# Kernel tuning notes

Measured on AMD Instinct MI355X. Metric: run time of the kernel, lower is better.

The kernel has to match this reference:

```python
import jax, jax.numpy as jnp
import numpy as np

KV_H, Q_H, ATT_H = 256, 256, 128
B, S, SQ = 2, 1024, 512

def setup_inputs() -> dict:
    key = jax.random.key(0)
    ks = jax.random.split(key, 8)
    sc = lambda d: 1.0 / np.sqrt(d)
    return {
        "attention_kv": jax.random.normal(ks[0], (B, S, KV_H), dtype=jnp.float32),
        "attention_query": jax.random.normal(ks[1], (B, SQ, Q_H), dtype=jnp.float32),
        "W_kv": jax.random.uniform(ks[2], (KV_H, ATT_H), jnp.float32, -sc(KV_H), sc(KV_H)),
        "b_kv": jax.random.uniform(ks[3], (ATT_H,), jnp.float32, -sc(KV_H), sc(KV_H)),
        "W_q": jax.random.uniform(ks[4], (Q_H, ATT_H), jnp.float32, -sc(Q_H), sc(Q_H)),
        "b_q": jax.random.uniform(ks[5], (ATT_H,), jnp.float32, -sc(Q_H), sc(Q_H)),
        "w_v": jax.random.uniform(ks[6], (ATT_H,), jnp.float32, -sc(ATT_H), sc(ATT_H)),
        "b_v": jax.random.uniform(ks[7], (), jnp.float32, -sc(ATT_H), sc(ATT_H)),
    }

def reference(attention_kv, attention_query, W_kv, b_kv, W_q, b_q, w_v, b_v):
    # proj_kv: (B, S, A); proj_q: (B, Sq, A)
    proj_kv = jnp.einsum('bsh,ha->bsa', attention_kv, W_kv) + b_kv
    proj_q = jnp.einsum('bqh,ha->bqa', attention_query, W_q) + b_q
    # broadcast add + tanh -> (B, Sq, S, A)
    hidden = jnp.tanh(proj_kv[:, None, :, :] + proj_q[:, :, None, :])
    # scalar score per (b, q, s)
    attention_score = jnp.einsum('bqsa,a->bqs', hidden, w_v) + b_v
    attention_weight = jax.nn.softmax(attention_score, axis=-1)
    # weighted sum over kv sequence -> (B, Sq, KV_H)
    attention_output = jnp.einsum('bqs,bsh->bqh', attention_weight, attention_kv)
    return attention_output, attention_weight
```

## Files before the change

### kernel.cpp

```cpp
#include <hip/hip_runtime.h>

#define NB   2
#define SKV  1024
#define NSQ  512
#define HIN  256
#define HA   128
#define NQ   (NB * NSQ)
#define NR   (NB * SKV)

#define KSC 2.8853900817779268f

typedef float v2f __attribute__((ext_vector_type(2)));
__device__ __forceinline__ v2f pkfma(v2f a, v2f b, v2f c) {
    return __builtin_elementwise_fma(a, b, c);
}

__global__ __launch_bounds__(256) void proj_kernel(
    const float* __restrict__ kv,  const float* __restrict__ qy,
    const float* __restrict__ Wkv, const float* __restrict__ bkv,
    const float* __restrict__ Wq,  const float* __restrict__ bq,
    float* __restrict__ ekT,
    float* __restrict__ eq)
{
    const int t = threadIdx.x;
    const int a = t & 127;
    const int g = __builtin_amdgcn_readfirstlane(t >> 7);
    const int blk = blockIdx.x;
    const bool is_q = blk >= 256;
    const int r0 = (is_q ? (blk - 256) : blk) * 8 + g * 4;
    const float* __restrict__ src = (is_q ? qy : kv) + (size_t)r0 * HIN;
    const float* __restrict__ W  = is_q ? Wq : Wkv;
    const float* __restrict__ bs = is_q ? bq : bkv;

    float ac0 = 0.f, ac1 = 0.f, ac2 = 0.f, ac3 = 0.f;
    #pragma unroll 8
    for (int h = 0; h < HIN; ++h) {
        const float w  = W[(size_t)h * HA + a];
        const float x0 = src[h];
        const float x1 = src[HIN + h];
        const float x2 = src[2 * HIN + h];
        const float x3 = src[3 * HIN + h];
        ac0 = fmaf(x0, w, ac0);
        ac1 = fmaf(x1, w, ac1);
        ac2 = fmaf(x2, w, ac2);
        ac3 = fmaf(x3, w, ac3);
    }
    const float bb = bs[a];
    const float o0 = __builtin_amdgcn_exp2f((ac0 + bb) * KSC);
    const float o1 = __builtin_amdgcn_exp2f((ac1 + bb) * KSC);
    const float o2 = __builtin_amdgcn_exp2f((ac2 + bb) * KSC);
    const float o3 = __builtin_amdgcn_exp2f((ac3 + bb) * KSC);
    if (!is_q) {
        float* __restrict__ d = ekT + (size_t)a * NR + r0;
        d[0] = o0; d[1] = o1; d[2] = o2; d[3] = o3;
    } else {
        eq[(size_t)(r0 + 0) * HA + a] = o0;
        eq[(size_t)(r0 + 1) * HA + a] = o1;
        eq[(size_t)(r0 + 2) * HA + a] = o2;
        eq[(size_t)(r0 + 3) * HA + a] = o3;
    }
}

__global__ __launch_bounds__(256) void score_kernel(
    const float* __restrict__ ekT,
    const float* __restrict__ eq,
    const float* __restrict__ wv,
    float* __restrict__ ew,
    float* __restrict__ ewT,
    float* __restrict__ Dp)
{
    __shared__ float dred[4][8];
    const int t = threadIdx.x;
    const int lane = t & 63, wid = t >> 6;
    const int blk = blockIdx.x;
    const int sq  = blk & 3;
    const int oct = blk >> 2;
    const int q0  = oct * 8;
    const int b   = q0 >> 9;
    const int s   = sq * 256 + t;
    const int srow = b * SKV + s;

    v2f acc[8];
    #pragma unroll
    for (int j = 0; j < 8; ++j) acc[j] = (v2f){0.f, 0.f};
    const v2f one = {1.f, 1.f};

    #pragma unroll 2
    for (int a4 = 0; a4 < 32; ++a4) {
        const float E0 = ekT[(size_t)(a4 * 4 + 0) * NR + srow];
        const float E1 = ekT[(size_t)(a4 * 4 + 1) * NR + srow];
        const float E2 = ekT[(size_t)(a4 * 4 + 2) * NR + srow];
        const float E3 = ekT[(size_t)(a4 * 4 + 3) * NR + srow];
        const float4 w4 = *(const float4*)(wv + a4 * 4);
        const v2f E01 = {E0, E1}, E23 = {E2, E3};
        const v2f w01 = {w4.x, w4.y}, w23 = {w4.z, w4.w};
        #pragma unroll
        for (int j = 0; j < 8; ++j) {
            const float4 qv = *(const float4*)(eq + (size_t)(q0 + j) * HA + a4 * 4);
            const v2f A = pkfma(E01, (v2f){qv.x, qv.y}, one);
            const v2f B = pkfma(E23, (v2f){qv.z, qv.w}, one);
            const v2f m = A * B;
            const float r = __builtin_amdgcn_rcpf(m.x * m.y);
            const v2f ts = (v2f){m.y, m.x} * (v2f){r, r};
            acc[j] = pkfma(w01, ts * B, acc[j]);
            acc[j] = pkfma(w23, ts * A, acc[j]);
        }
    }

    float ev[8];
    #pragma unroll
    for (int j = 0; j < 8; ++j) {
        ev[j] = __builtin_amdgcn_exp2f(-KSC * (acc[j].x + acc[j].y));
        ew[(size_t)(q0 + j) * SKV + s] = ev[j];
    }
    {
        float* __restrict__ wp = ewT + ((size_t)oct * SKV + s) * 8;
        *(float4*)(wp)     = make_float4(ev[0], ev[1], ev[2], ev[3]);
        *(float4*)(wp + 4) = make_float4(ev[4], ev[5], ev[6], ev[7]);
    }
    #pragma unroll
    for (int j = 0; j < 8; ++j) {
        float ss = ev[j];
        #pragma unroll
        for (int o = 32; o > 0; o >>= 1) ss += __shfl_down(ss, o);
        if (lane == 0) dred[wid][j] = ss;
    }
    __syncthreads();
    if (t < 8) {
        float d = dred[0][t] + dred[1][t] + dred[2][t] + dred[3][t];
        Dp[(size_t)sq * NQ + q0 + t] = d;
    }
}

__global__ __launch_bounds__(512) void out_kernel(
    const float* __restrict__ ewT,
    const float* __restrict__ kv,
    float* __restrict__ P)
{
    const int t = threadIdx.x;
    const int lane = t & 63;
    const int wu = __builtin_amdgcn_readfirstlane(t >> 6);
    const int blk = blockIdx.x;
    const int k  = blk & 3;
    const int gi = blk >> 2;
    const int q0 = gi * 16;
    const int b  = q0 >> 9;
    const int o0 = q0 >> 3;

    v2f acc[16][2];
    #pragma unroll
    for (int j = 0; j < 16; ++j) { acc[j][0] = (v2f){0.f, 0.f}; acc[j][1] = (v2f){0.f, 0.f}; }

    const int sbase = k * 256 + wu * 32;
    const float* __restrict__ kvb = kv + ((size_t)b * SKV + sbase) * HIN + lane * 4;
    const float* __restrict__ wA = ewT + ((size_t)o0 * SKV + sbase) * 8;
    const float* __restrict__ wB = ewT + ((size_t)(o0 + 1) * SKV + sbase) * 8;

    #pragma unroll 4
    for (int i = 0; i < 32; ++i) {
        const float4 v = *(const float4*)(kvb + (size_t)i * HIN);
        const v2f vlo = {v.x, v.y}, vhi = {v.z, v.w};
        const float4 a0 = *(const float4*)(wA + (size_t)i * 8);
        const float4 a1 = *(const float4*)(wA + (size_t)i * 8 + 4);
        const float4 b0 = *(const float4*)(wB + (size_t)i * 8);
        const float4 b1 = *(const float4*)(wB + (size_t)i * 8 + 4);
        const float wq[16] = {a0.x, a0.y, a0.z, a0.w, a1.x, a1.y, a1.z, a1.w,
                              b0.x, b0.y, b0.z, b0.w, b1.x, b1.y, b1.z, b1.w};
        #pragma unroll
        for (int j = 0; j < 16; ++j) {
            const v2f wj = {wq[j], wq[j]};
            acc[j][0] = pkfma(vlo, wj, acc[j][0]);
            acc[j][1] = pkfma(vhi, wj, acc[j][1]);
        }
    }
    float* __restrict__ Pp = P + (size_t)(k * 8 + wu) * ((size_t)NQ * HIN);
    #pragma unroll
    for (int j = 0; j < 16; ++j) {
        *(float4*)(Pp + (size_t)(q0 + j) * HIN + lane * 4) =
            make_float4(acc[j][0].x, acc[j][0].y, acc[j][1].x, acc[j][1].y);
    }
}

__global__ __launch_bounds__(256) void final_kernel(
    const float* __restrict__ ew,
    const float* __restrict__ Dp,
    const float* __restrict__ P,
    float* __restrict__ out)
{
    const int t = threadIdx.x;
    const int q = blockIdx.x;
    const float D = Dp[q] + Dp[NQ + q] + Dp[2 * NQ + q] + Dp[3 * NQ + q];
    const float rw = 1.0f / D;

    float* __restrict__ outw = out + (size_t)NQ * HIN;
    #pragma unroll
    for (int c = 0; c < 4; ++c) {
        const int s = c * 256 + t;
        outw[(size_t)q * SKV + s] = ew[(size_t)q * SKV + s] * rw;
    }
    float v = 0.f;
    #pragma unroll
    for (int p = 0; p < 32; ++p)
        v += P[(size_t)p * ((size_t)NQ * HIN) + (size_t)q * HIN + t];
    out[(size_t)q * HIN + t] = v * rw;
}

extern "C" void kernel_launch(void* const* d_in, const int* in_sizes, int n_in,
                              void* d_out, int out_size, void* d_ws, size_t ws_size,
                              hipStream_t stream) {
    (void)in_sizes; (void)n_in; (void)out_size; (void)ws_size;
    const float* kv  = (const float*)d_in[0];
    const float* qy  = (const float*)d_in[1];
    const float* Wkv = (const float*)d_in[2];
    const float* bkv = (const float*)d_in[3];
    const float* Wq  = (const float*)d_in[4];
    const float* bq  = (const float*)d_in[5];
    const float* wv  = (const float*)d_in[6];
    const float* bv  = (const float*)d_in[7];
    (void)bv;

    float* ekT = (float*)d_ws;
    float* eq  = ekT + 262144;
    float* ew  = eq  + 131072;
    float* ewT = ew  + 1048576;
    float* Dp  = ewT + 1048576;
    float* P   = Dp  + 4096;
    float* out = (float*)d_out;

    hipLaunchKernelGGL(proj_kernel,  dim3(384),  dim3(256), 0, stream,
                       kv, qy, Wkv, bkv, Wq, bq, ekT, eq);
    hipLaunchKernelGGL(score_kernel, dim3(512),  dim3(256), 0, stream,
                       ekT, eq, wv, ew, ewT, Dp);
    hipLaunchKernelGGL(out_kernel,   dim3(256),  dim3(512), 0, stream,
                       ewT, kv, P);
    hipLaunchKernelGGL(final_kernel, dim3(1024), dim3(256), 0, stream,
                       ew, Dp, P, out);
}
```

Before: 129.4 us.

## Fuse four attention stages into one cooperative kernel with grid syncs

Replaces the four separate launches (projection, score, weighted sum, final reduction) with a single cooperative kernel of 256 blocks of 1024 threads that uses grid.sync between phases. The work split is also reorganized: projection splits the hidden reduction across thread groups and combines the halves in shared memory, and the output stage reduces partials in shared memory so only two partial slices are written instead of thirty-two. The aim is to cut launch gaps and partial-sum traffic, at the cost of grid-wide barriers and only 256 large blocks, which may leave the GPU underoccupied.

```diff
diff --git a/kernel.cpp b/kernel.cpp
--- a/kernel.cpp
+++ b/kernel.cpp
@@ -1,12 +1,13 @@
 #include <hip/hip_runtime.h>
-
-#define NB   2
+#include <hip/hip_cooperative_groups.h>
+namespace cg = cooperative_groups;
+
 #define SKV  1024
 #define NSQ  512
 #define HIN  256
 #define HA   128
-#define NQ   (NB * NSQ)
-#define NR   (NB * SKV)
+#define NQ   1024
+#define NR   2048
 
 #define KSC 2.8853900817779268f
 
@@ -15,194 +16,213 @@
     return __builtin_elementwise_fma(a, b, c);
 }
 
-__global__ __launch_bounds__(256) void proj_kernel(
+__global__ __launch_bounds__(1024, 4) void fused_kernel(
     const float* __restrict__ kv,  const float* __restrict__ qy,
     const float* __restrict__ Wkv, const float* __restrict__ bkv,
     const float* __restrict__ Wq,  const float* __restrict__ bq,
+    const float* __restrict__ wv,
     float* __restrict__ ekT,
-    float* __restrict__ eq)
-{
-    const int t = threadIdx.x;
-    const int a = t & 127;
-    const int g = __builtin_amdgcn_readfirstlane(t >> 7);
-    const int blk = blockIdx.x;
-    const bool is_q = blk >= 256;
-    const int r0 = (is_q ? (blk - 256) : blk) * 8 + g * 4;
-    const float* __restrict__ src = (is_q ? qy : kv) + (size_t)r0 * HIN;
-    const float* __restrict__ W  = is_q ? Wq : Wkv;
-    const float* __restrict__ bs = is_q ? bq : bkv;
-
-    float ac0 = 0.f, ac1 = 0.f, ac2 = 0.f, ac3 = 0.f;
-    #pragma unroll 8
-    for (int h = 0; h < HIN; ++h) {
-        const float w  = W[(size_t)h * HA + a];
-        const float x0 = src[h];
-        const float x1 = src[HIN + h];
-        const float x2 = src[2 * HIN + h];
-        const float x3 = src[3 * HIN + h];
-        ac0 = fmaf(x0, w, ac0);
-        ac1 = fmaf(x1, w, ac1);
-        ac2 = fmaf(x2, w, ac2);
-        ac3 = fmaf(x3, w, ac3);
-    }
-    const float bb = bs[a];
-    const float o0 = __builtin_amdgcn_exp2f((ac0 + bb) * KSC);
-    const float o1 = __builtin_amdgcn_exp2f((ac1 + bb) * KSC);
-    const float o2 = __builtin_amdgcn_exp2f((ac2 + bb) * KSC);
-    const float o3 = __builtin_amdgcn_exp2f((ac3 + bb) * KSC);
-    if (!is_q) {
-        float* __restrict__ d = ekT + (size_t)a * NR + r0;
-        d[0] = o0; d[1] = o1; d[2] = o2; d[3] = o3;
-    } else {
-        eq[(size_t)(r0 + 0) * HA + a] = o0;
-        eq[(size_t)(r0 + 1) * HA + a] = o1;
-        eq[(size_t)(r0 + 2) * HA + a] = o2;
-        eq[(size_t)(r0 + 3) * HA + a] = o3;
-    }
-}
-
-__global__ __launch_bounds__(256) void score_kernel(
-    const float* __restrict__ ekT,
-    const float* __restrict__ eq,
-    const float* __restrict__ wv,
+    float* __restrict__ eq,
     float* __restrict__ ew,
     float* __restrict__ ewT,
-    float* __restrict__ Dp)
-{
-    __shared__ float dred[4][8];
-    const int t = threadIdx.x;
-    const int lane = t & 63, wid = t >> 6;
-    const int blk = blockIdx.x;
-    const int sq  = blk & 3;
-    const int oct = blk >> 2;
-    const int q0  = oct * 8;
-    const int b   = q0 >> 9;
-    const int s   = sq * 256 + t;
-    const int srow = b * SKV + s;
-
-    v2f acc[8];
-    #pragma unroll
-    for (int j = 0; j < 8; ++j) acc[j] = (v2f){0.f, 0.f};
-    const v2f one = {1.f, 1.f};
-
-    #pragma unroll 2
-    for (int a4 = 0; a4 < 32; ++a4) {
-        const float E0 = ekT[(size_t)(a4 * 4 + 0) * NR + srow];
-        const float E1 = ekT[(size_t)(a4 * 4 + 1) * NR + srow];
-        const float E2 = ekT[(size_t)(a4 * 4 + 2) * NR + srow];
-        const float E3 = ekT[(size_t)(a4 * 4 + 3) * NR + srow];
-        const float4 w4 = *(const float4*)(wv + a4 * 4);
-        const v2f E01 = {E0, E1}, E23 = {E2, E3};
-        const v2f w01 = {w4.x, w4.y}, w23 = {w4.z, w4.w};
-        #pragma unroll
-        for (int j = 0; j < 8; ++j) {
-            const float4 qv = *(const float4*)(eq + (size_t)(q0 + j) * HA + a4 * 4);
-            const v2f A = pkfma(E01, (v2f){qv.x, qv.y}, one);
-            const v2f B = pkfma(E23, (v2f){qv.z, qv.w}, one);
-            const v2f m = A * B;
-            const float r = __builtin_amdgcn_rcpf(m.x * m.y);
-            const v2f ts = (v2f){m.y, m.x} * (v2f){r, r};
-            acc[j] = pkfma(w01, ts * B, acc[j]);
-            acc[j] = pkfma(w23, ts * A, acc[j]);
-        }
-    }
-
-    float ev[8];
-    #pragma unroll
-    for (int j = 0; j < 8; ++j) {
-        ev[j] = __builtin_amdgcn_exp2f(-KSC * (acc[j].x + acc[j].y));
-        ew[(size_t)(q0 + j) * SKV + s] = ev[j];
-    }
-    {
-        float* __restrict__ wp = ewT + ((size_t)oct * SKV + s) * 8;
-        *(float4*)(wp)     = make_float4(ev[0], ev[1], ev[2], ev[3]);
-        *(float4*)(wp + 4) = make_float4(ev[4], ev[5], ev[6], ev[7]);
-    }
-    #pragma unroll
-    for (int j = 0; j < 8; ++j) {
-        float ss = ev[j];
-        #pragma unroll
-        for (int o = 32; o > 0; o >>= 1) ss += __shfl_down(ss, o);
-        if (lane == 0) dred[wid][j] = ss;
-    }
-    __syncthreads();
-    if (t < 8) {
-        float d = dred[0][t] + dred[1][t] + dred[2][t] + dred[3][t];
-        Dp[(size_t)sq * NQ + q0 + t] = d;
-    }
-}
-
-__global__ __launch_bounds__(512) void out_kernel(
-    const float* __restrict__ ewT,
-    const float* __restrict__ kv,
-    float* __restrict__ P)
-{
-    const int t = threadIdx.x;
-    const int lane = t & 63;
-    const int wu = __builtin_amdgcn_readfirstlane(t >> 6);
-    const int blk = blockIdx.x;
-    const int k  = blk & 3;
-    const int gi = blk >> 2;
-    const int q0 = gi * 16;
-    const int b  = q0 >> 9;
-    const int o0 = q0 >> 3;
-
-    v2f acc[16][2];
-    #pragma unroll
-    for (int j = 0; j < 16; ++j) { acc[j][0] = (v2f){0.f, 0.f}; acc[j][1] = (v2f){0.f, 0.f}; }
-
-    const int sbase = k * 256 + wu * 32;
-    const float* __restrict__ kvb = kv + ((size_t)b * SKV + sbase) * HIN + lane * 4;
-    const float* __restrict__ wA = ewT + ((size_t)o0 * SKV + sbase) * 8;
-    const float* __restrict__ wB = ewT + ((size_t)(o0 + 1) * SKV + sbase) * 8;
-
-    #pragma unroll 4
-    for (int i = 0; i < 32; ++i) {
-        const float4 v = *(const float4*)(kvb + (size_t)i * HIN);
-        const v2f vlo = {v.x, v.y}, vhi = {v.z, v.w};
-        const float4 a0 = *(const float4*)(wA + (size_t)i * 8);
-        const float4 a1 = *(const float4*)(wA + (size_t)i * 8 + 4);
-        const float4 b0 = *(const float4*)(wB + (size_t)i * 8);
-        const float4 b1 = *(const float4*)(wB + (size_t)i * 8 + 4);
-        const float wq[16] = {a0.x, a0.y, a0.z, a0.w, a1.x, a1.y, a1.z, a1.w,
-                              b0.x, b0.y, b0.z, b0.w, b1.x, b1.y, b1.z, b1.w};
-        #pragma unroll
-        for (int j = 0; j < 16; ++j) {
-            const v2f wj = {wq[j], wq[j]};
-            acc[j][0] = pkfma(vlo, wj, acc[j][0]);
-            acc[j][1] = pkfma(vhi, wj, acc[j][1]);
-        }
-    }
-    float* __restrict__ Pp = P + (size_t)(k * 8 + wu) * ((size_t)NQ * HIN);
-    #pragma unroll
-    for (int j = 0; j < 16; ++j) {
-        *(float4*)(Pp + (size_t)(q0 + j) * HIN + lane * 4) =
-            make_float4(acc[j][0].x, acc[j][0].y, acc[j][1].x, acc[j][1].y);
-    }
-}
-
-__global__ __launch_bounds__(256) void final_kernel(
-    const float* __restrict__ ew,
-    const float* __restrict__ Dp,
-    const float* __restrict__ P,
+    float* __restrict__ Dp,
+    float* __restrict__ P2,
     float* __restrict__ out)
 {
-    const int t = threadIdx.x;
-    const int q = blockIdx.x;
-    const float D = Dp[q] + Dp[NQ + q] + Dp[2 * NQ + q] + Dp[3 * NQ + q];
-    const float rw = 1.0f / D;
-
-    float* __restrict__ outw = out + (size_t)NQ * HIN;
-    #pragma unroll
-    for (int c = 0; c < 4; ++c) {
-        const int s = c * 256 + t;
-        outw[(size_t)q * SKV + s] = ew[(size_t)q * SKV + s] * rw;
-    }
-    float v = 0.f;
-    #pragma unroll
-    for (int p = 0; p < 32; ++p)
-        v += P[(size_t)p * ((size_t)NQ * HIN) + (size_t)q * HIN + t];
-    out[(size_t)q * HIN + t] = v * rw;
+    cg::grid_group grid = cg::this_grid();
+    __shared__ float smem[8 * 16 * 128];
+    const int t    = threadIdx.x;
+    const int blk  = blockIdx.x;
+    const int lane = t & 63;
+    const int w    = t >> 6;
+
+    {
+        const int a = t & 127;
+        const int g = __builtin_amdgcn_readfirstlane(t >> 7);
+        if (g < 4) {
+            const int role = g >> 1;
+            const int gh   = g & 1;
+            const float* __restrict__ W = (role ? Wq : Wkv) + (size_t)gh * 128 * HA;
+            const float* __restrict__ src = (role ? (qy + (size_t)blk * 4 * HIN)
+                                                  : (kv + (size_t)blk * 8 * HIN)) + gh * 128;
+            if (role == 0) {
+                float ac[8] = {0,0,0,0,0,0,0,0};
+                #pragma unroll 4
+                for (int h = 0; h < 128; ++h) {
+                    const float wl = W[(size_t)h * HA + a];
+                    #pragma unroll
+                    for (int r = 0; r < 8; ++r)
+                        ac[r] = fmaf(src[(size_t)r * HIN + h], wl, ac[r]);
+                }
+                #pragma unroll
+                for (int r = 0; r < 8; ++r) smem[(gh * 12 + r) * 128 + a] = ac[r];
+            } else {
+                float ac[4] = {0,0,0,0};
+                #pragma unroll 4
+                for (int h = 0; h < 128; ++h) {
+                    const float wl = W[(size_t)h * HA + a];
+                    #pragma unroll
+                    for (int r = 0; r < 4; ++r)
+                        ac[r] = fmaf(src[(size_t)r * HIN + h], wl, ac[r]);
+                }
+                #pragma unroll
+                for (int r = 0; r < 4; ++r) smem[(gh * 12 + 8 + r) * 128 + a] = ac[r];
+            }
+        }
+        __syncthreads();
+        #pragma unroll
+        for (int id = t; id < 1536; id += 1024) {
+            const int r = id >> 7, a2 = id & 127;
+            const float v  = smem[r * 128 + a2] + smem[(12 + r) * 128 + a2];
+            const bool isq = r >= 8;
+            const float bb = (isq ? bq : bkv)[a2];
+            const float o  = __builtin_amdgcn_exp2f((v + bb) * KSC);
+            if (!isq) ekT[(size_t)a2 * NR + blk * 8 + r] = o;
+            else      eq[((size_t)blk * 4 + (r - 8)) * HA + a2] = o;
+        }
+    }
+    grid.sync();
+
+    {
+        const int oct = blk >> 1, sh = blk & 1;
+        const int q0  = oct * 8;
+        const int b   = q0 >> 9;
+        const int qh  = __builtin_amdgcn_readfirstlane(t >> 9);
+        const int s   = sh * 512 + (t & 511);
+        const int srow = b * SKV + s;
+
+        v2f acc[4];
+        #pragma unroll
+        for (int j = 0; j < 4; ++j) acc[j] = (v2f){0.f, 0.f};
+        const v2f one = {1.f, 1.f};
+
+        #pragma unroll 2
+        for (int a4 = 0; a4 < 32; ++a4) {
+            const float E0 = ekT[(size_t)(a4 * 4 + 0) * NR + srow];
+            const float E1 = ekT[(size_t)(a4 * 4 + 1) * NR + srow];
+            const float E2 = ekT[(size_t)(a4 * 4 + 2) * NR + srow];
+            const float E3 = ekT[(size_t)(a4 * 4 + 3) * NR + srow];
+            const float4 w4 = *(const float4*)(wv + a4 * 4);
+            const v2f E01 = {E0, E1}, E23 = {E2, E3};
+            const v2f w01 = {w4.x, w4.y}, w23 = {w4.z, w4.w};
+            #pragma unroll
+            for (int j = 0; j < 4; ++j) {
+                const float4 qv = *(const float4*)(eq + ((size_t)q0 + qh * 4 + j) * HA + a4 * 4);
+                const v2f A = pkfma(E01, (v2f){qv.x, qv.y}, one);
+                const v2f B = pkfma(E23, (v2f){qv.z, qv.w}, one);
+                const v2f m = A * B;
+                const float r = __builtin_amdgcn_rcpf(m.x * m.y);
+                const v2f ts = (v2f){m.y, m.x} * (v2f){r, r};
+                acc[j] = pkfma(w01, ts * B, acc[j]);
+                acc[j] = pkfma(w23, ts * A, acc[j]);
+            }
+        }
+        float ev[4];
+        #pragma unroll
+        for (int j = 0; j < 4; ++j) {
+            ev[j] = __builtin_amdgcn_exp2f(-KSC * (acc[j].x + acc[j].y));
+            ew[((size_t)q0 + qh * 4 + j) * SKV + s] = ev[j];
+        }
+        *(float4*)(ewT + ((size_t)oct * SKV + s) * 8 + qh * 4) =
+            make_float4(ev[0], ev[1], ev[2], ev[3]);
+
+        float* dred = smem;
+        #pragma unroll
+        for (int j = 0; j < 4; ++j) {
+            float ssum = ev[j];
+            #pragma unroll
+            for (int o = 32; o > 0; o >>= 1) ssum += __shfl_down(ssum, o);
+            if (lane == 0) dred[w * 4 + j] = ssum;
+        }
+        __syncthreads();
+        if ((t & 511) < 4) {
+            const int j = t & 3;
+            const int base = qh * 32;
+            float d = 0.f;
+            #pragma unroll
+            for (int k = 0; k < 8; ++k) d += dred[base + k * 4 + j];
+            Dp[(size_t)sh * NQ + q0 + qh * 4 + j] = d;
+        }
+    }
+    grid.sync();
+
+    {
+        const int gi  = blk >> 2;
+        const int hh  = (blk >> 1) & 1;
+        const int sh  = blk & 1;
+        const int q0g = gi * 16;
+        const int b   = q0g >> 9;
+        const int o0  = gi * 2;
+
+        if (hh == 0) {
+            const int jh = __builtin_amdgcn_readfirstlane(t >> 9);
+            const int s  = sh * 512 + (t & 511);
+            float* __restrict__ outw = out + (size_t)NQ * HIN;
+            #pragma unroll
+            for (int jj = 0; jj < 8; ++jj) {
+                const int qq = q0g + jh * 8 + jj;
+                const float D = Dp[qq] + Dp[NQ + qq];
+                outw[(size_t)qq * SKV + s] =
+                    ew[(size_t)qq * SKV + s] * __builtin_amdgcn_rcpf(D);
+            }
+        }
+
+        const int sbase = sh * 512 + w * 32;
+        const float* __restrict__ kvp =
+            kv + ((size_t)(b * SKV + sbase)) * HIN + hh * 128 + lane * 2;
+        const float* __restrict__ wA = ewT + ((size_t)o0 * SKV + sbase) * 8;
+        const float* __restrict__ wB = ewT + ((size_t)(o0 + 1) * SKV + sbase) * 8;
+
+        v2f acc[16];
+        #pragma unroll
+        for (int j = 0; j < 16; ++j) acc[j] = (v2f){0.f, 0.f};
+        #pragma unroll 2
+        for (int i = 0; i < 32; ++i) {
+            const v2f v = *(const v2f*)(kvp + (size_t)i * HIN);
+            const float4 a0 = *(const float4*)(wA + i * 8);
+            const float4 a1 = *(const float4*)(wA + i * 8 + 4);
+            const float4 b0 = *(const float4*)(wB + i * 8);
+            const float4 b1 = *(const float4*)(wB + i * 8 + 4);
+            const float wq[16] = {a0.x, a0.y, a0.z, a0.w, a1.x, a1.y, a1.z, a1.w,
+                                  b0.x, b0.y, b0.z, b0.w, b1.x, b1.y, b1.z, b1.w};
+            #pragma unroll
+            for (int j = 0; j < 16; ++j)
+                acc[j] = pkfma(v, (v2f){wq[j], wq[j]}, acc[j]);
+        }
+        float* part = smem;
+        if (w < 8) {
+            #pragma unroll
+            for (int j = 0; j < 16; ++j)
+                *(v2f*)(part + ((size_t)w * 16 + j) * 128 + lane * 2) = acc[j];
+        }
+        __syncthreads();
+        if (w >= 8) {
+            #pragma unroll
+            for (int j = 0; j < 16; ++j) {
+                v2f* p = (v2f*)(part + ((size_t)(w - 8) * 16 + j) * 128 + lane * 2);
+                *p = *p + acc[j];
+            }
+        }
+        __syncthreads();
+        #pragma unroll
+        for (int k = 0; k < 2; ++k) {
+            const int id = t + k * 1024;
+            const int j = id >> 7, hl = id & 127;
+            const int qq = q0g + j;
+            float vs = 0.f;
+            #pragma unroll
+            for (int gg = 0; gg < 8; ++gg) vs += part[((size_t)gg * 16 + j) * 128 + hl];
+            const float D = Dp[qq] + Dp[NQ + qq];
+            P2[(size_t)sh * ((size_t)NQ * HIN) + (size_t)qq * HIN + hh * 128 + hl] =
+                vs * __builtin_amdgcn_rcpf(D);
+        }
+    }
+    grid.sync();
+
+    {
+        const size_t idx = (size_t)blk * 1024 + t;
+        out[idx] = P2[idx] + P2[(size_t)NQ * HIN + idx];
+    }
 }
 
 extern "C" void kernel_launch(void* const* d_in, const int* in_sizes, int n_in,
@@ -216,23 +236,19 @@
     const float* Wq  = (const float*)d_in[4];
     const float* bq  = (const float*)d_in[5];
     const float* wv  = (const float*)d_in[6];
-    const float* bv  = (const float*)d_in[7];
-    (void)bv;
 
     float* ekT = (float*)d_ws;
     float* eq  = ekT + 262144;
     float* ew  = eq  + 131072;
     float* ewT = ew  + 1048576;
     float* Dp  = ewT + 1048576;
-    float* P   = Dp  + 4096;
+    float* P2  = Dp  + 2048;
     float* out = (float*)d_out;
 
-    hipLaunchKernelGGL(proj_kernel,  dim3(384),  dim3(256), 0, stream,
-                       kv, qy, Wkv, bkv, Wq, bq, ekT, eq);
-    hipLaunchKernelGGL(score_kernel, dim3(512),  dim3(256), 0, stream,
-                       ekT, eq, wv, ew, ewT, Dp);
-    hipLaunchKernelGGL(out_kernel,   dim3(256),  dim3(512), 0, stream,
-                       ewT, kv, P);
-    hipLaunchKernelGGL(final_kernel, dim3(1024), dim3(256), 0, stream,
-                       ew, Dp, P, out);
+    void* args[] = { (void*)&kv, (void*)&qy, (void*)&Wkv, (void*)&bkv,
+                     (void*)&Wq, (void*)&bq, (void*)&wv,
+                     (void*)&ekT, (void*)&eq, (void*)&ew, (void*)&ewT,
+                     (void*)&Dp, (void*)&P2, (void*)&out };
+    hipLaunchCooperativeKernel((const void*)fused_kernel, dim3(256), dim3(1024),
+                               args, 0, stream);
 }
```

Result: slower. 234.6 us (+81.3%).
